# Performance work log

Measured on AMD Instinct MI355X. Metric: run time of the kernel, lower is better.

## Reference

```python
import jax, jax.numpy as jnp
import numpy as np

EPS = 1e-6

def _complex_linear(xr, xi, wr, wi):
    # torch Linear: y = x @ W.T ; complex: (xr+i*xi)(Wr+i*Wi)
    yr = jnp.einsum('bsd,ed->bse', xr, wr) - jnp.einsum('bsd,ed->bse', xi, wi)
    yi = jnp.einsum('bsd,ed->bse', xr, wi) + jnp.einsum('bsd,ed->bse', xi, wr)
    return yr, yi

def setup_inputs() -> dict:
    key = jax.random.key(0)
    ks = jax.random.split(key, 12)
    B, S, D = 32768, 16, 64
    inp = {
        'z_real': jax.random.normal(ks[0], (B, D), jnp.float32),
        'z_imag': jax.random.normal(ks[1], (B, D), jnp.float32),
        'mem':    jax.random.normal(ks[2], (B, S, 2 * D), jnp.float32),
        'ptr':    jax.random.uniform(ks[3], (B, S), jnp.float32),
        'ctrl':   jax.random.normal(ks[4], (B, 3), jnp.float32),
        'wq_r': jax.random.normal(ks[5], (D, D), jnp.float32) / np.sqrt(D),
        'wq_i': jax.random.normal(ks[6], (D, D), jnp.float32) / np.sqrt(D),
        'wk_r': jax.random.normal(ks[7], (D, D), jnp.float32) / np.sqrt(D),
        'wk_i': jax.random.normal(ks[8], (D, D), jnp.float32) / np.sqrt(D),
        'wv_r': jax.random.normal(ks[9], (D, D), jnp.float32) / np.sqrt(D),
        'wv_i': jax.random.normal(ks[10], (D, D), jnp.float32) / np.sqrt(D),
    }
    return inp

def reference(z_real, z_imag, mem, ptr, ctrl, wq_r, wq_i, wk_r, wk_i, wv_r, wv_i):
    D = z_real.shape[-1]
    # soft push/pop/stay gates, normalized
    g = jax.nn.sigmoid(ctrl)  # (B,3)
    push, pop, stay = g[:, 0:1], g[:, 1:2], g[:, 2:3]
    total = push + pop + stay + EPS
    push, pop, stay = push / total, pop / total, stay / total
    # pointer update via rolls
    ptr_up = jnp.roll(ptr, 1, axis=1)
    ptr_down = jnp.roll(ptr, -1, axis=1)
    new_ptr = push * ptr_up + pop * ptr_down + stay * ptr  # (B,S)
    # memory write
    z_flat = jnp.concatenate([z_real, z_imag], axis=-1)  # (B,2D)
    mem_new = mem * (1.0 - push[..., None]) + push[..., None] * z_flat[:, None, :]
    mr, mi = mem_new[..., :D], mem_new[..., D:]  # (B,S,D) complex memory
    # complex attention over stack slots
    qr, qi = _complex_linear(mr, mi, wq_r, wq_i)
    kr, ki = _complex_linear(mr, mi, wk_r, wk_i)
    vr, vi = _complex_linear(mr, mi, wv_r, wv_i)
    q_flat = jnp.concatenate([qr, qi], axis=-1)  # (B,S,2D)
    k_flat = jnp.concatenate([kr, ki], axis=-1)
    scale = D ** (-0.5)
    scores = jnp.einsum('bse,bte->bst', q_flat, k_flat) * scale  # (B,S,S)
    attn = jax.nn.softmax(scores, axis=-1)
    ar = jnp.einsum('bst,btd->bsd', attn, vr)
    ai = jnp.einsum('bst,btd->bsd', attn, vi)
    att_flat = jnp.concatenate([ar, ai], axis=-1)  # (B,S,2D)
    # pointer-weighted read
    read_flat = (att_flat * new_ptr[..., None]).sum(axis=1)  # (B,2D)
    z_read_r, z_read_i = read_flat[:, :D], read_flat[:, D:]
    active_slots = (new_ptr > 0.1).astype(jnp.float32).sum(axis=1).mean()
    return (z_read_r, z_read_i, mem_new, new_ptr, active_slots)
```

## Files before the change

### kernel.cpp

```cpp
#include <hip/hip_runtime.h>


typedef __bf16 bf16x8 __attribute__((ext_vector_type(8)));
typedef float  f32x4  __attribute__((ext_vector_type(4)));
typedef float  f4     __attribute__((ext_vector_type(4)));

#define B_TOT   32768
#define GRID_WG 512
#define NWAVES  4096
#define BPW     8
#define LOG2E   1.4426950408889634f
#define EXSC    0.18033688011112042f

__device__ __forceinline__ unsigned short f2bf(float x) {
  __bf16 h = (__bf16)x;
  return __builtin_bit_cast(unsigned short, h);
}
__device__ __forceinline__ float rcp_f(float x) { return __builtin_amdgcn_rcpf(x); }
__device__ __forceinline__ float ex2_f(float x) { return __builtin_amdgcn_exp2f(x); }
__device__ __forceinline__ float sigm(float x) { return rcp_f(1.0f + ex2_f(-LOG2E * x)); }

__device__ __forceinline__ float dpp_sum16(float v) {
  int x;
  x = __builtin_amdgcn_update_dpp(0, __builtin_bit_cast(int, v), 0xB1, 0xF, 0xF, false);
  v += __builtin_bit_cast(float, x);
  x = __builtin_amdgcn_update_dpp(0, __builtin_bit_cast(int, v), 0x4E, 0xF, 0xF, false);
  v += __builtin_bit_cast(float, x);
  x = __builtin_amdgcn_update_dpp(0, __builtin_bit_cast(int, v), 0x141, 0xF, 0xF, false);
  v += __builtin_bit_cast(float, x);
  x = __builtin_amdgcn_update_dpp(0, __builtin_bit_cast(int, v), 0x140, 0xF, 0xF, false);
  v += __builtin_bit_cast(float, x);
  return v;
}

__global__ void ems_fin(const unsigned int* __restrict__ c, float* __restrict__ out) {
  if (threadIdx.x == 0) out[0] = (float)(*c) * (1.0f / 32768.0f);
}

__global__ void __launch_bounds__(128)
ems_mt(const float* __restrict__ wqr, const float* __restrict__ wqi,
       const float* __restrict__ wkr, const float* __restrict__ wki,
       unsigned short* __restrict__ mt, unsigned int* __restrict__ cnt)
{
  if (blockIdx.x == 0 && threadIdx.x == 0) *cnt = 0u;
  __shared__ float sK[128];
  const int e2 = (int)blockIdx.x;
  const int e  = (int)threadIdx.x;
  float kv;
  if (e < 64) kv = (e2 < 64) ? wkr[e*64 + e2]      : -wki[e*64 + (e2-64)];
  else        kv = (e2 < 64) ? wki[(e-64)*64 + e2] :  wkr[(e-64)*64 + (e2-64)];
  sK[e] = kv;
  __syncthreads();
  float acc = 0.0f;
  #pragma unroll 8
  for (int Ep = 0; Ep < 64; ++Ep) {
    float q = (e < 64) ? wqr[Ep*64 + e] : -wqi[Ep*64 + (e-64)];
    acc += q * sK[Ep];
  }
  #pragma unroll 8
  for (int Ep = 0; Ep < 64; ++Ep) {
    float q = (e < 64) ? wqi[Ep*64 + e] : wqr[Ep*64 + (e-64)];
    acc += q * sK[64 + Ep];
  }
  mt[e2*128 + e] = f2bf(acc);
}

__global__ void __launch_bounds__(512, 4)
ems_main(const float* __restrict__ z_real, const float* __restrict__ z_imag,
         const float* __restrict__ mem,    const float* __restrict__ ptrv,
         const float* __restrict__ ctrl,
         const float* __restrict__ wvr,    const float* __restrict__ wvi,
         const unsigned short* __restrict__ mt,
         float* __restrict__ out_zr, float* __restrict__ out_zi,
         float* __restrict__ out_mem, float* __restrict__ out_ptr,
         unsigned int* __restrict__ ws_cnt)
{
  __shared__ __align__(16) unsigned short lds[40960];

  const int tid = (int)threadIdx.x;

  for (int idx = tid; idx < 16384; idx += 512) {
    int e2 = idx >> 7, e = idx & 127;
    lds[(e2 << 7) + (((e >> 3) ^ (e2 & 15)) << 3) + (e & 7)] = mt[idx];
  }
  #pragma unroll
  for (int m = 0; m < 2; ++m) {
    const float* wp = m ? wvi : wvr;
    for (int idx = tid; idx < 4096; idx += 512) {
      int e = idx >> 6, d = idx & 63;
      lds[16384 + (m << 12) + (e << 6) + (((d >> 3) ^ (e & 7)) << 3) + (d & 7)] = f2bf(wp[idx]);
    }
  }
  __syncthreads();

  const int lane = tid & 63;
  const int wv   = tid >> 6;
  const int c    = lane & 15;
  const int g    = lane >> 4;

  {
    int phase = (wv << 1) | (((int)blockIdx.x >> 8) & 1);
    #pragma unroll 1
    for (int i = 0; i < phase; ++i) __builtin_amdgcn_s_sleep(44);
  }

  unsigned short* SY = &lds[24576 + (wv << 11)];

  const f4* mem4 = (const f4*)mem;
  const f4* zr4  = (const f4*)z_real;
  const f4* zi4  = (const f4*)z_imag;
  f4* omem4 = (f4*)out_mem;

  unsigned int active_acc = 0u;
  const int b0 = (int)blockIdx.x * 8 + wv;

  for (int it = 0; it < BPW; ++it) {
    const int b = b0 + it * NWAVES;

    f4 cm[8], cz[8];
    #pragma unroll
    for (int t4 = 0; t4 < 4; ++t4) {
      int i4 = b*512 + c*32 + t4*8 + g*2;
      cm[2*t4]   = mem4[i4];
      cm[2*t4+1] = mem4[i4+1];
    }
    {
      int zb = b*16 + g*2;
      cz[0] = zr4[zb];   cz[1] = zr4[zb+1];
      cz[2] = zr4[zb+8]; cz[3] = zr4[zb+9];
      cz[4] = zi4[zb];   cz[5] = zi4[zb+1];
      cz[6] = zi4[zb+8]; cz[7] = zi4[zb+9];
    }

    float pu = sigm(ctrl[b*3+0]);
    float po = sigm(ctrl[b*3+1]);
    float st = sigm(ctrl[b*3+2]);
    float rt = rcp_f(pu + po + st + 1e-6f);
    pu *= rt; po *= rt; st *= rt;

    float pm = ptrv[b*16 + ((c+15)&15)];
    float pp = ptrv[b*16 + ((c+ 1)&15)];
    float pc = ptrv[b*16 + c];
    float np = pu*pm + po*pp + st*pc;
    if (g == 0) out_ptr[b*16 + c] = np;
    unsigned long long ball = __ballot(np > 0.1f);
    active_acc += (unsigned int)__popcll(ball & 0xFFFFull);

    float om = 1.0f - pu;
    bf16x8 af[4], afn[2];
    #pragma unroll
    for (int t4 = 0; t4 < 4; ++t4) {
      f4 r0 = cm[2*t4]   * om + pu * cz[2*t4];
      f4 r1 = cm[2*t4+1] * om + pu * cz[2*t4+1];
      int i4 = b*512 + c*32 + t4*8 + g*2;
      omem4[i4]   = r0;
      omem4[i4+1] = r1;
      #pragma unroll
      for (int k = 0; k < 4; ++k) {
        af[t4][k]   = (__bf16)r0[k];
        af[t4][4+k] = (__bf16)r1[k];
      }
      if (t4 >= 2) {
        #pragma unroll
        for (int k = 0; k < 4; ++k) {
          afn[t4-2][k]   = (__bf16)(-r0[k]);
          afn[t4-2][4+k] = (__bf16)(-r1[k]);
        }
      }
    }

    #pragma unroll
    for (int n2 = 0; n2 < 8; ++n2) {
      int e2 = (n2 << 4) + c;
      f32x4 acc = {0.f,0.f,0.f,0.f};
      #pragma unroll
      for (int T = 0; T < 4; ++T) {
        bf16x8 am = *(const bf16x8*)&lds[(e2 << 7) + ((((T << 2) + g) ^ c) << 3)];
        acc = __builtin_amdgcn_mfma_f32_16x16x32_bf16(am, af[T], acc, 0, 0, 0);
      }
      uint2 pk;
      pk.x = (unsigned)f2bf(acc[0]) | ((unsigned)f2bf(acc[1]) << 16);
      pk.y = (unsigned)f2bf(acc[2]) | ((unsigned)f2bf(acc[3]) << 16);
      *(uint2*)&SY[(c << 7) + ((((n2 << 1) + (g >> 1)) ^ c) << 3) + ((g & 1) << 2)] = pk;
    }

    f32x4 sc = {0.f,0.f,0.f,0.f};
    #pragma unroll
    for (int T = 0; T < 4; ++T) {
      bf16x8 yb = *(const bf16x8*)&SY[(c << 7) + ((((T << 2) + g) ^ c) << 3)];
      sc = __builtin_amdgcn_mfma_f32_16x16x32_bf16(af[T], yb, sc, 0, 0, 0);
    }

    float e0 = ex2_f(sc[0] * EXSC);
    float e1 = ex2_f(sc[1] * EXSC);
    float e2v = ex2_f(sc[2] * EXSC);
    float e3 = ex2_f(sc[3] * EXSC);
    float r = (e0 + e1) + (e2v + e3);
    r += __shfl_xor(r, 16, 64);
    r += __shfl_xor(r, 32, 64);
    float u = np * rcp_f(r);
    float w4[4];
    w4[0] = dpp_sum16(u * e0);
    w4[1] = dpp_sum16(u * e1);
    w4[2] = dpp_sum16(u * e2v);
    w4[3] = dpp_sum16(u * e3);

    #pragma unroll
    for (int n = 0; n < 4; ++n) {
      int eb = 16384 + (((n << 4) + c) << 6);
      int e7 = c & 7;
      f32x4 ar = {0.f,0.f,0.f,0.f}, ai = {0.f,0.f,0.f,0.f};
      #pragma unroll
      for (int t = 0; t < 2; ++t) {
        int ch = (((t << 2) + g) ^ e7) << 3;
        bf16x8 fr = *(const bf16x8*)&lds[eb + ch];
        bf16x8 fi = *(const bf16x8*)&lds[eb + 4096 + ch];
        ar = __builtin_amdgcn_mfma_f32_16x16x32_bf16(af[t],   fr, ar, 0,0,0);
        ai = __builtin_amdgcn_mfma_f32_16x16x32_bf16(af[t],   fi, ai, 0,0,0);
        ar = __builtin_amdgcn_mfma_f32_16x16x32_bf16(afn[t],  fi, ar, 0,0,0);
        ai = __builtin_amdgcn_mfma_f32_16x16x32_bf16(af[t+2], fr, ai, 0,0,0);
      }
      float prr = ar[0]*w4[0] + ar[1]*w4[1] + ar[2]*w4[2] + ar[3]*w4[3];
      float pri = ai[0]*w4[0] + ai[1]*w4[1] + ai[2]*w4[2] + ai[3]*w4[3];
      prr += __shfl_xor(prr, 16, 64);
      prr += __shfl_xor(prr, 32, 64);
      pri += __shfl_xor(pri, 16, 64);
      pri += __shfl_xor(pri, 32, 64);
      if (g == 0) out_zr[b*64 + (n << 4) + c] = prr;
      if (g == 1) out_zi[b*64 + (n << 4) + c] = pri;
    }
  }

  __syncthreads();
  unsigned int* cnt_lds = (unsigned int*)&lds[24576];
  if (tid == 0) *cnt_lds = 0u;
  __syncthreads();
  if (lane == 0) atomicAdd(cnt_lds, active_acc);
  __syncthreads();
  if (tid == 0) atomicAdd(ws_cnt, *cnt_lds);
}

extern "C" void kernel_launch(void* const* d_in, const int* in_sizes, int n_in,
                              void* d_out, int out_size, void* d_ws, size_t ws_size,
                              hipStream_t stream) {
  const float* z_real = (const float*)d_in[0];
  const float* z_imag = (const float*)d_in[1];
  const float* memp   = (const float*)d_in[2];
  const float* ptrv   = (const float*)d_in[3];
  const float* ctrl   = (const float*)d_in[4];
  const float* wq_r   = (const float*)d_in[5];
  const float* wq_i   = (const float*)d_in[6];
  const float* wk_r   = (const float*)d_in[7];
  const float* wk_i   = (const float*)d_in[8];
  const float* wv_r   = (const float*)d_in[9];
  const float* wv_i   = (const float*)d_in[10];

  float* out     = (float*)d_out;
  float* out_zr  = out;
  float* out_zi  = out + 2097152;
  float* out_mem = out + 4194304;
  float* out_ptr = out + 71303168;
  float* out_sc  = out + 71827456;

  unsigned int*   cnt = (unsigned int*)d_ws;
  unsigned short* mtp = (unsigned short*)((char*)d_ws + 1024);

  ems_mt<<<128, 128, 0, stream>>>(wq_r, wq_i, wk_r, wk_i, mtp, cnt);
  ems_main<<<GRID_WG, 512, 0, stream>>>(z_real, z_imag, memp, ptrv, ctrl,
                                        wv_r, wv_i, mtp,
                                        out_zr, out_zi, out_mem, out_ptr, cnt);
  ems_fin<<<1, 64, 0, stream>>>(cnt, out_sc);
}
```

Baseline: 147.9 us.

## Coalesce mem/z loads and reshuffle MFMA operands through LDS

Mem rows are now loaded with lane-contiguous f4 accesses, so each load instruction covers a contiguous 1KB span, and z is fetched as a single f4 per lane. The updated memory is staged as bf16 into the per-wave LDS scratch and read back in the MFMA operand layout. Negated operands are built by flipping bf16 sign bits instead of converting again. This trades strided global access for an extra LDS round trip and reuses the SY buffer before the later writes.

```diff
diff --git a/kernel.cpp b/kernel.cpp
--- a/kernel.cpp
+++ b/kernel.cpp
@@ -19,6 +19,12 @@
 __device__ __forceinline__ float rcp_f(float x) { return __builtin_amdgcn_rcpf(x); }
 __device__ __forceinline__ float ex2_f(float x) { return __builtin_amdgcn_exp2f(x); }
 __device__ __forceinline__ float sigm(float x) { return rcp_f(1.0f + ex2_f(-LOG2E * x)); }
+
+__device__ __forceinline__ bf16x8 negbf8(bf16x8 v) {
+  uint4 u = __builtin_bit_cast(uint4, v);
+  u.x ^= 0x80008000u; u.y ^= 0x80008000u; u.z ^= 0x80008000u; u.w ^= 0x80008000u;
+  return __builtin_bit_cast(bf16x8, u);
+}
 
 __device__ __forceinline__ float dpp_sum16(float v) {
   int x;
@@ -97,6 +103,7 @@
   const int wv   = tid >> 6;
   const int c    = lane & 15;
   const int g    = lane >> 4;
+  const int d4   = lane & 31;
 
   {
     int phase = (wv << 1) | (((int)blockIdx.x >> 8) & 1);
@@ -117,20 +124,10 @@
   for (int it = 0; it < BPW; ++it) {
     const int b = b0 + it * NWAVES;
 
-    f4 cm[8], cz[8];
-    #pragma unroll
-    for (int t4 = 0; t4 < 4; ++t4) {
-      int i4 = b*512 + c*32 + t4*8 + g*2;
-      cm[2*t4]   = mem4[i4];
-      cm[2*t4+1] = mem4[i4+1];
-    }
-    {
-      int zb = b*16 + g*2;
-      cz[0] = zr4[zb];   cz[1] = zr4[zb+1];
-      cz[2] = zr4[zb+8]; cz[3] = zr4[zb+9];
-      cz[4] = zi4[zb];   cz[5] = zi4[zb+1];
-      cz[6] = zi4[zb+8]; cz[7] = zi4[zb+9];
-    }
+    f4 cm[8];
+    #pragma unroll
+    for (int k = 0; k < 8; ++k) cm[k] = mem4[b*512 + (k << 6) + lane];
+    f4 z4 = (d4 < 16) ? zr4[b*16 + d4] : zi4[b*16 + (d4 - 16)];
 
     float pu = sigm(ctrl[b*3+0]);
     float po = sigm(ctrl[b*3+1]);
@@ -147,27 +144,23 @@
     active_acc += (unsigned int)__popcll(ball & 0xFFFFull);
 
     float om = 1.0f - pu;
+    #pragma unroll
+    for (int k = 0; k < 8; ++k) {
+      f4 r = cm[k] * om + pu * z4;
+      omem4[b*512 + (k << 6) + lane] = r;
+      uint2 pk;
+      pk.x = (unsigned)f2bf(r[0]) | ((unsigned)f2bf(r[1]) << 16);
+      pk.y = (unsigned)f2bf(r[2]) | ((unsigned)f2bf(r[3]) << 16);
+      int row = (k << 1) + (lane >> 5);
+      *(uint2*)&SY[(row << 7) + (((d4 >> 1) ^ row) << 3) + ((d4 & 1) << 2)] = pk;
+    }
+
     bf16x8 af[4], afn[2];
     #pragma unroll
-    for (int t4 = 0; t4 < 4; ++t4) {
-      f4 r0 = cm[2*t4]   * om + pu * cz[2*t4];
-      f4 r1 = cm[2*t4+1] * om + pu * cz[2*t4+1];
-      int i4 = b*512 + c*32 + t4*8 + g*2;
-      omem4[i4]   = r0;
-      omem4[i4+1] = r1;
-      #pragma unroll
-      for (int k = 0; k < 4; ++k) {
-        af[t4][k]   = (__bf16)r0[k];
-        af[t4][4+k] = (__bf16)r1[k];
-      }
-      if (t4 >= 2) {
-        #pragma unroll
-        for (int k = 0; k < 4; ++k) {
-          afn[t4-2][k]   = (__bf16)(-r0[k]);
-          afn[t4-2][4+k] = (__bf16)(-r1[k]);
-        }
-      }
-    }
+    for (int t = 0; t < 4; ++t)
+      af[t] = *(const bf16x8*)&SY[(c << 7) + ((((t << 2) + g) ^ c) << 3)];
+    afn[0] = negbf8(af[2]);
+    afn[1] = negbf8(af[3]);
 
     #pragma unroll
     for (int n2 = 0; n2 < 8; ++n2) {
```

After: 146.3 us. Within noise of the previous version (-1.1%).
